# Kernel tuning notes

Hardware: AMD Instinct MI355X
Metric: run time of the kernel (lower is better)

Reference implementation:

```python
import jax, jax.numpy as jnp
import numpy as np

N_NODES = 100000
EPS = 1e-5


def _layernorm(x, gamma, beta):
    mu = jnp.mean(x, axis=-1, keepdims=True)
    var = jnp.mean(jnp.square(x - mu), axis=-1, keepdims=True)
    return (x - mu) * jax.lax.rsqrt(var + EPS) * gamma + beta


def _gcn_layer(src, dst, feat, gamma, beta, W, b):
    # copy_u + sum: aggregate source features into destination nodes
    agg = jax.ops.segment_sum(feat[src], dst, num_segments=N_NODES)
    h = _layernorm(agg, gamma, beta)
    return h @ W + b


def setup_inputs() -> dict:
    key = jax.random.key(0)
    ks = jax.random.split(key, 16)
    d_in, d_hid, d_out = 128, 128, 128
    E = 1600000

    def lin(k, fan_in, fan_out):
        kw, kb = jax.random.split(k)
        lim = 1.0 / np.sqrt(fan_in)
        W = jax.random.uniform(kw, (fan_in, fan_out), jnp.float32, -lim, lim)
        b = jax.random.uniform(kb, (fan_out,), jnp.float32, -lim, lim)
        return W, b

    W1, b1 = lin(ks[0], d_in, d_hid)
    W2, b2 = lin(ks[1], d_hid, d_hid)
    W3, b3 = lin(ks[2], d_hid, d_out)
    return {
        "features": jax.random.normal(ks[3], (N_NODES, d_in), jnp.float32),
        "src": jax.random.randint(ks[4], (E,), 0, N_NODES, jnp.int32),
        "dst": jax.random.randint(ks[5], (E,), 0, N_NODES, jnp.int32),
        "g1": jnp.ones((d_in,), jnp.float32), "be1": jnp.zeros((d_in,), jnp.float32),
        "W1": W1, "b1": b1,
        "g2": jnp.ones((d_hid,), jnp.float32), "be2": jnp.zeros((d_hid,), jnp.float32),
        "W2": W2, "b2": b2,
        "g3": jnp.ones((d_hid,), jnp.float32), "be3": jnp.zeros((d_hid,), jnp.float32),
        "W3": W3, "b3": b3,
    }


def reference(features, src, dst, g1, be1, W1, b1, g2, be2, W2, b2, g3, be3, W3, b3):
    x = jax.nn.relu(_gcn_layer(src, dst, features, g1, be1, W1, b1))
    x = jax.nn.relu(_gcn_layer(src, dst, x, g2, be2, W2, b2))
    x = _gcn_layer(src, dst, x, g3, be3, W3, b3)
    return x
```

## Files before the change

kernel.cpp:

```cpp
#include <hip/hip_runtime.h>
#include <hip/hip_bf16.h>
#include <stdint.h>

typedef unsigned short u16;
typedef __attribute__((ext_vector_type(8))) short short8;
typedef __attribute__((ext_vector_type(4))) float f32x4;

#define DIM 128
#define CAP 64

__device__ __forceinline__ float bflo(uint32_t v) {
    uint32_t b = v << 16;
    float f; __builtin_memcpy(&f, &b, 4); return f;
}
__device__ __forceinline__ float bfhi(uint32_t v) {
    uint32_t b = v & 0xffff0000u;
    float f; __builtin_memcpy(&f, &b, 4); return f;
}
__device__ __forceinline__ u16 f2bf(float f) {
    uint32_t x; __builtin_memcpy(&x, &f, 4);
    uint32_t r = (x + 0x7fffu + ((x >> 16) & 1u)) >> 16;
    return (u16)r;
}
__device__ __forceinline__ uint32_t pack2bf(float a, float b) {
    return (uint32_t)f2bf(a) | ((uint32_t)f2bf(b) << 16);
}


__global__ __launch_bounds__(256) void k_bin1(
    const int* __restrict__ src, const int* __restrict__ dst,
    uint32_t* __restrict__ gCur, uint32_t* __restrict__ groupBuf,
    int E, int ngrp, int gcap)
{
    __shared__ uint32_t hcnt[512];
    __shared__ uint32_t hbase[512];
    __shared__ uint32_t hcur[512];
    int nb = gridDim.x;
    int per = (E + nb - 1) / nb;
    int lo = blockIdx.x * per;
    int hi = lo + per; if (hi > E) hi = E;

    for (int t = threadIdx.x; t < ngrp; t += 256) { hcnt[t] = 0; hcur[t] = 0; }
    __syncthreads();

    for (int i = lo + threadIdx.x; i < hi; i += 256)
        atomicAdd(&hcnt[((uint32_t)dst[i]) >> 8], 1u);
    __syncthreads();

    int rot = (blockIdx.x * 37) % (ngrp > 0 ? ngrp : 1);
    for (int k = threadIdx.x; k < ngrp; k += 256) {
        int t = k + rot; if (t >= ngrp) t -= ngrp;
        uint32_t c = hcnt[t];
        hbase[t] = c ? atomicAdd(&gCur[t], c) : 0u;
    }
    __syncthreads();

    for (int i = lo + threadIdx.x; i < hi; i += 256) {
        uint32_t d = (uint32_t)dst[i];
        uint32_t g = d >> 8;
        uint32_t off = hbase[g] + atomicAdd(&hcur[g], 1u);
        if (off < (uint32_t)gcap)
            groupBuf[(size_t)g * gcap + off] = (uint32_t)src[i] | ((d & 255u) << 20);
    }
}

__global__ __launch_bounds__(256) void k_bin2(
    const uint32_t* __restrict__ groupBuf, const uint32_t* __restrict__ gCur,
    uint32_t* __restrict__ bucket, uint32_t* __restrict__ cnt,
    int N, int gcap)
{
    __shared__ uint32_t ncur[256];
    int g = blockIdx.x;
    ncur[threadIdx.x] = 0;
    __syncthreads();
    uint32_t m = gCur[g]; if (m > (uint32_t)gcap) m = gcap;
    int nodebase = g << 8;
    const uint32_t* buf = groupBuf + (size_t)g * gcap;
    for (uint32_t i = threadIdx.x; i < m; i += 256) {
        uint32_t v = buf[i];
        uint32_t nl = v >> 20;
        uint32_t s = v & 0xFFFFFu;
        uint32_t pos = atomicAdd(&ncur[nl], 1u);
        if (pos < CAP) bucket[(size_t)(nodebase + (int)nl) * CAP + pos] = s;
    }
    __syncthreads();
    int node = nodebase + threadIdx.x;
    if (node < N) cnt[node] = ncur[threadIdx.x];
}


__global__ void k_cast(const float* __restrict__ in, uint32_t* __restrict__ out, int n4) {
    int i = blockIdx.x * blockDim.x + threadIdx.x;
    int stride = gridDim.x * blockDim.x;
    const float4* in4 = (const float4*)in;
    uint2* out2 = (uint2*)out;
    for (; i < n4; i += stride) {
        float4 v = in4[i];
        uint2 r;
        r.x = pack2bf(v.x, v.y);
        r.y = pack2bf(v.z, v.w);
        out2[i] = r;
    }
}


__global__ void k_zero_row(uint32_t* __restrict__ a, uint32_t* __restrict__ b, int N) {
    int t = threadIdx.x;
    if (t < 64) a[(size_t)N * 64 + t] = 0u;
    else        b[(size_t)N * 64 + (t - 64)] = 0u;
}


__global__ void k_transpose3(const float* __restrict__ w0, const float* __restrict__ w1,
                             const float* __restrict__ w2, u16* __restrict__ t0,
                             u16* __restrict__ t1, u16* __restrict__ t2) {
    const float* w = blockIdx.x == 0 ? w0 : (blockIdx.x == 1 ? w1 : w2);
    u16* o = blockIdx.x == 0 ? t0 : (blockIdx.x == 1 ? t1 : t2);
    for (int idx = threadIdx.x; idx < DIM * DIM; idx += blockDim.x) {
        int r = idx >> 7, c = idx & 127;
        o[c * DIM + r] = f2bf(w[idx]);
    }
}


__global__ __launch_bounds__(256) void k_gather_ln(
    const uint32_t* __restrict__ xin, const uint32_t* __restrict__ cnt,
    const uint32_t* __restrict__ bucket,
    const int* __restrict__ src, const int* __restrict__ dst,
    const float* __restrict__ gamma, const float* __restrict__ beta,
    uint32_t* __restrict__ h, int N, int E)
{
    int w = threadIdx.x >> 6, l = threadIdx.x & 63;
    int node = __builtin_amdgcn_readfirstlane(blockIdx.x * 4 + w);
    if (node >= N) return;
    uint32_t c = cnt[node];
    float a0 = 0.f, a1 = 0.f;

    if (__builtin_expect(c > CAP, 0)) {
        for (int e = 0; e < E; ++e) {
            if (dst[e] == node) {
                uint32_t v = xin[(size_t)src[e] * 64 + l];
                a0 += bflo(v); a1 += bfhi(v);
            }
        }
    } else {
        uint32_t bktv = bucket[(size_t)node * CAP + l];
#pragma unroll
        for (int g = 0; g < 4; ++g) {
            if ((uint32_t)(g * 16 + 16) <= c) {
                uint32_t v[16];
#pragma unroll
                for (int i = 0; i < 16; ++i) {
                    const int SLOT = g * 16 + i;
                    uint32_t su = (uint32_t)__builtin_amdgcn_readfirstlane(
                        (int)((uint32_t)__builtin_amdgcn_readlane(bktv, SLOT)));
                    v[i] = (xin + (size_t)su * 64)[l];
                }
#pragma unroll
                for (int i = 0; i < 16; ++i) { a0 += bflo(v[i]); a1 += bfhi(v[i]); }
            } else if ((uint32_t)(g * 16) < c) {
                uint32_t v[16];
#pragma unroll
                for (int q = 0; q < 4; ++q) {
                    if ((uint32_t)(g * 16 + q * 4) < c) {
#pragma unroll
                        for (int i = 0; i < 4; ++i) {
                            const int SLOT = g * 16 + q * 4 + i;
                            uint32_t su = (uint32_t)__builtin_amdgcn_readfirstlane(
                                (int)((uint32_t)__builtin_amdgcn_readlane(bktv, SLOT)));
                            su = ((uint32_t)SLOT < c) ? su : (uint32_t)N;
                            v[q * 4 + i] = (xin + (size_t)su * 64)[l];
                        }
                    }
                }
#pragma unroll
                for (int q = 0; q < 4; ++q) {
                    if ((uint32_t)(g * 16 + q * 4) < c) {
#pragma unroll
                        for (int i = 0; i < 4; ++i) {
                            a0 += bflo(v[q * 4 + i]); a1 += bfhi(v[q * 4 + i]);
                        }
                    }
                }
            }
        }
    }

    float sum = a0 + a1;
    float sq  = a0 * a0 + a1 * a1;
    for (int off = 32; off; off >>= 1) {
        sum += __shfl_xor(sum, off, 64);
        sq  += __shfl_xor(sq,  off, 64);
    }
    float mean = sum * (1.f / 128.f);
    float var  = sq * (1.f / 128.f) - mean * mean;
    float rs   = rsqrtf(var + 1e-5f);
    float g0 = gamma[2 * l], g1 = gamma[2 * l + 1];
    float b0 = beta[2 * l],  b1 = beta[2 * l + 1];
    float h0 = (a0 - mean) * rs * g0 + b0;
    float h1 = (a1 - mean) * rs * g1 + b1;
    h[(size_t)node * 64 + l] = pack2bf(h0, h1);
}


template <int RELU, int OUTF32>
__global__ __launch_bounds__(256) void k_gemm(
    const u16* __restrict__ h, const u16* __restrict__ wt,
    const float* __restrict__ bias, void* __restrict__ outp, int N)
{
    int w = threadIdx.x >> 6, l = threadIdx.x & 63;
    int colbase = (w >> 1) * 64;
    int lr = l & 15, lg = l >> 4;

    short8 bfrag[4][4];
    float bv[4];
#pragma unroll
    for (int ct = 0; ct < 4; ++ct) {
        bv[ct] = bias[colbase + ct * 16 + lr];
#pragma unroll
        for (int kc = 0; kc < 4; ++kc)
            bfrag[ct][kc] = *(const short8*)(wt + (size_t)(colbase + ct * 16 + lr) * DIM + kc * 32 + lg * 8);
    }

    int ntiles = (N + 31) / 32;
    int t = blockIdx.x;
    if (t >= ntiles) return;

    auto loadA = [&](int tt, short8* af) {
        int ar = tt * 32 + 16 * (w & 1) + lr;
        if (ar > N - 1) ar = N - 1;
#pragma unroll
        for (int kc = 0; kc < 4; ++kc)
            af[kc] = *(const short8*)(h + (size_t)ar * DIM + kc * 32 + lg * 8);
    };

    short8 afrag[4];
    loadA(t, afrag);

    while (true) {
        int tn = t + (int)gridDim.x;
        bool has = tn < ntiles;
        short8 anext[4];
        if (has) loadA(tn, anext);

        int row0 = t * 32 + 16 * (w & 1);
#pragma unroll
        for (int ct = 0; ct < 4; ++ct) {
            f32x4 a = {0.f, 0.f, 0.f, 0.f};
#pragma unroll
            for (int kc = 0; kc < 4; ++kc)
                a = __builtin_amdgcn_mfma_f32_16x16x32_bf16(afrag[kc], bfrag[ct][kc], a, 0, 0, 0);
            int col = colbase + ct * 16 + lr;
#pragma unroll
            for (int j = 0; j < 4; ++j) {
                int row = row0 + lg * 4 + j;
                float v = a[j] + bv[ct];
                if (RELU) v = fmaxf(v, 0.f);
                if (row < N) {
                    if (OUTF32) ((float*)outp)[(size_t)row * DIM + col] = v;
                    else        ((u16*)outp)[(size_t)row * DIM + col] = f2bf(v);
                }
            }
        }

        if (!has) break;
#pragma unroll
        for (int kc = 0; kc < 4; ++kc) afrag[kc] = anext[kc];
        t = tn;
    }
}


extern "C" void kernel_launch(void* const* d_in, const int* in_sizes, int n_in,
                              void* d_out, int out_size, void* d_ws, size_t ws_size,
                              hipStream_t stream) {
    const float* feat = (const float*)d_in[0];
    const int* src  = (const int*)d_in[1];
    const int* dst  = (const int*)d_in[2];
    const float* g1 = (const float*)d_in[3],  *be1 = (const float*)d_in[4];
    const float* W1 = (const float*)d_in[5],  *b1  = (const float*)d_in[6];
    const float* g2 = (const float*)d_in[7],  *be2 = (const float*)d_in[8];
    const float* W2 = (const float*)d_in[9],  *b2  = (const float*)d_in[10];
    const float* g3 = (const float*)d_in[11], *be3 = (const float*)d_in[12];
    const float* W3 = (const float*)d_in[13], *b3  = (const float*)d_in[14];

    int N = in_sizes[0] / DIM;
    int E = in_sizes[1];
    float* out = (float*)d_out;

    int ngrp = (N + 255) >> 8;
    int gcap = (E / (ngrp > 0 ? ngrp : 1)) * 3 / 2 + 1024;

    char* ws = (char*)d_ws;
    auto alloc = [&](size_t bytes) {
        char* p = ws;
        ws += (bytes + 255) & ~(size_t)255;
        return p;
    };
    uint32_t* gCur     = (uint32_t*)alloc((size_t)ngrp * 4);
    uint32_t* groupBuf = (uint32_t*)alloc((size_t)ngrp * gcap * 4);
    uint32_t* cnt      = (uint32_t*)alloc((size_t)N * 4);
    uint32_t* bucket   = (uint32_t*)alloc((size_t)N * CAP * 4);
    u16* wt1 = (u16*)alloc(DIM * DIM * 2);
    u16* wt2 = (u16*)alloc(DIM * DIM * 2);
    u16* wt3 = (u16*)alloc(DIM * DIM * 2);
    uint32_t* X0 = (uint32_t*)alloc((size_t)(N + 1) * 64 * 4);
    uint32_t* H  = (uint32_t*)alloc((size_t)(N + 1) * 64 * 4);
    uint32_t* X  = (uint32_t*)alloc((size_t)(N + 1) * 64 * 4);

    hipMemsetAsync(gCur, 0, (size_t)ngrp * 4, stream);
    k_bin1<<<256, 256, 0, stream>>>(src, dst, gCur, groupBuf, E, ngrp, gcap);
    k_bin2<<<ngrp, 256, 0, stream>>>(groupBuf, gCur, bucket, cnt, N, gcap);
    k_transpose3<<<3, 256, 0, stream>>>(W1, W2, W3, wt1, wt2, wt3);
    k_cast<<<1024, 256, 0, stream>>>(feat, X0, N * 32);
    k_zero_row<<<1, 128, 0, stream>>>(X0, X, N);

    int gblocks = (N + 3) / 4;

    k_gather_ln<<<gblocks, 256, 0, stream>>>(X0, cnt, bucket, src, dst, g1, be1, H, N, E);
    k_gemm<1, 0><<<512, 256, 0, stream>>>((const u16*)H, wt1, b1, X, N);
    k_gather_ln<<<gblocks, 256, 0, stream>>>(X, cnt, bucket, src, dst, g2, be2, H, N, E);
    k_gemm<1, 0><<<512, 256, 0, stream>>>((const u16*)H, wt2, b2, X, N);
    k_gather_ln<<<gblocks, 256, 0, stream>>>(X, cnt, bucket, src, dst, g3, be3, H, N, E);
    k_gemm<0, 1><<<512, 256, 0, stream>>>((const u16*)H, wt3, b3, out, N);
}
```

Before: 310.0 us.

## Process two nodes per wavefront in gather-LN and merge prep kernels

The gather+layernorm kernel now has each wavefront aggregate two destination nodes, issuing two independent sets of gathers to raise memory-level parallelism. The warp reductions for both nodes are interleaved. The tail handling is simplified to always issue 16 loads per group, with unused slots redirected to the zero row. The weight-transpose, cast and zero-row kernels are fused into one prep launch to cut launch overhead, and k_bin1 gets twice as many blocks. The risks are higher register pressure, fewer waves in flight, and wasted loads on partial groups.

```diff
diff --git a/kernel.cpp b/kernel.cpp
--- a/kernel.cpp
+++ b/kernel.cpp
@@ -89,36 +89,37 @@
 }
 
 
-__global__ void k_cast(const float* __restrict__ in, uint32_t* __restrict__ out, int n4) {
-    int i = blockIdx.x * blockDim.x + threadIdx.x;
-    int stride = gridDim.x * blockDim.x;
-    const float4* in4 = (const float4*)in;
-    uint2* out2 = (uint2*)out;
-    for (; i < n4; i += stride) {
-        float4 v = in4[i];
-        uint2 r;
-        r.x = pack2bf(v.x, v.y);
-        r.y = pack2bf(v.z, v.w);
-        out2[i] = r;
-    }
-}
-
-
-__global__ void k_zero_row(uint32_t* __restrict__ a, uint32_t* __restrict__ b, int N) {
-    int t = threadIdx.x;
-    if (t < 64) a[(size_t)N * 64 + t] = 0u;
-    else        b[(size_t)N * 64 + (t - 64)] = 0u;
-}
-
-
-__global__ void k_transpose3(const float* __restrict__ w0, const float* __restrict__ w1,
-                             const float* __restrict__ w2, u16* __restrict__ t0,
-                             u16* __restrict__ t1, u16* __restrict__ t2) {
-    const float* w = blockIdx.x == 0 ? w0 : (blockIdx.x == 1 ? w1 : w2);
-    u16* o = blockIdx.x == 0 ? t0 : (blockIdx.x == 1 ? t1 : t2);
-    for (int idx = threadIdx.x; idx < DIM * DIM; idx += blockDim.x) {
-        int r = idx >> 7, c = idx & 127;
-        o[c * DIM + r] = f2bf(w[idx]);
+__global__ void k_prep(const float* __restrict__ feat, uint32_t* __restrict__ X0,
+                       uint32_t* __restrict__ X, int N,
+                       const float* __restrict__ W1, const float* __restrict__ W2,
+                       const float* __restrict__ W3,
+                       u16* __restrict__ t0, u16* __restrict__ t1, u16* __restrict__ t2)
+{
+    int b = blockIdx.x;
+    if (b < 3) {
+        const float* w = b == 0 ? W1 : (b == 1 ? W2 : W3);
+        u16* o = b == 0 ? t0 : (b == 1 ? t1 : t2);
+        for (int idx = threadIdx.x; idx < DIM * DIM; idx += blockDim.x) {
+            int r = idx >> 7, c = idx & 127;
+            o[c * DIM + r] = f2bf(w[idx]);
+        }
+    } else if (b == 3) {
+        int t = threadIdx.x;
+        if (t < 64) X0[(size_t)N * 64 + t] = 0u;
+        else if (t < 128) X[(size_t)N * 64 + (t - 64)] = 0u;
+    } else {
+        int n4 = N * 32;
+        int i = (b - 4) * 256 + threadIdx.x;
+        int stride = (gridDim.x - 4) * 256;
+        const float4* in4 = (const float4*)feat;
+        uint2* out2 = (uint2*)X0;
+        for (; i < n4; i += stride) {
+            float4 v = in4[i];
+            uint2 r;
+            r.x = pack2bf(v.x, v.y);
+            r.y = pack2bf(v.z, v.w);
+            out2[i] = r;
+        }
     }
 }
 
@@ -131,75 +132,85 @@
     uint32_t* __restrict__ h, int N, int E)
 {
     int w = threadIdx.x >> 6, l = threadIdx.x & 63;
-    int node = __builtin_amdgcn_readfirstlane(blockIdx.x * 4 + w);
-    if (node >= N) return;
-    uint32_t c = cnt[node];
-    float a0 = 0.f, a1 = 0.f;
-
-    if (__builtin_expect(c > CAP, 0)) {
+    int node0 = __builtin_amdgcn_readfirstlane(2 * (blockIdx.x * 4 + w));
+    if (node0 >= N) return;
+    int node1 = node0 + 1;
+    bool has1 = node1 < N;
+    uint32_t c0 = cnt[node0];
+    uint32_t c1 = has1 ? cnt[node1] : 0u;
+    float a0 = 0.f, a1 = 0.f, b0 = 0.f, b1 = 0.f;
+
+    if (__builtin_expect(c0 > CAP || c1 > CAP, 0)) {
         for (int e = 0; e < E; ++e) {
-            if (dst[e] == node) {
-                uint32_t v = xin[(size_t)src[e] * 64 + l];
-                a0 += bflo(v); a1 += bfhi(v);
-            }
+            int d = dst[e];
+            if (d == node0) { uint32_t v = xin[(size_t)src[e] * 64 + l]; a0 += bflo(v); a1 += bfhi(v); }
+            else if (d == node1) { uint32_t v = xin[(size_t)src[e] * 64 + l]; b0 += bflo(v); b1 += bfhi(v); }
         }
     } else {
-        uint32_t bktv = bucket[(size_t)node * CAP + l];
-#pragma unroll
-        for (int g = 0; g < 4; ++g) {
-            if ((uint32_t)(g * 16 + 16) <= c) {
-                uint32_t v[16];
-#pragma unroll
-                for (int i = 0; i < 16; ++i) {
-                    const int SLOT = g * 16 + i;
-                    uint32_t su = (uint32_t)__builtin_amdgcn_readfirstlane(
-                        (int)((uint32_t)__builtin_amdgcn_readlane(bktv, SLOT)));
-                    v[i] = (xin + (size_t)su * 64)[l];
-                }
-#pragma unroll
-                for (int i = 0; i < 16; ++i) { a0 += bflo(v[i]); a1 += bfhi(v[i]); }
-            } else if ((uint32_t)(g * 16) < c) {
-                uint32_t v[16];
-#pragma unroll
-                for (int q = 0; q < 4; ++q) {
-                    if ((uint32_t)(g * 16 + q * 4) < c) {
-#pragma unroll
-                        for (int i = 0; i < 4; ++i) {
-                            const int SLOT = g * 16 + q * 4 + i;
-                            uint32_t su = (uint32_t)__builtin_amdgcn_readfirstlane(
-                                (int)((uint32_t)__builtin_amdgcn_readlane(bktv, SLOT)));
-                            su = ((uint32_t)SLOT < c) ? su : (uint32_t)N;
-                            v[q * 4 + i] = (xin + (size_t)su * 64)[l];
-                        }
+        {
+            uint32_t bktv = bucket[(size_t)node0 * CAP + l];
+#pragma unroll
+            for (int g = 0; g < 4; ++g) {
+                if ((uint32_t)(g * 16) < c0) {
+                    uint32_t v[16];
+#pragma unroll
+                    for (int i = 0; i < 16; ++i) {
+                        const int SLOT = g * 16 + i;
+                        uint32_t su = (uint32_t)__builtin_amdgcn_readfirstlane(
+                            (int)((uint32_t)__builtin_amdgcn_readlane(bktv, SLOT)));
+                        su = ((uint32_t)SLOT < c0) ? su : (uint32_t)N;
+                        v[i] = (xin + (size_t)su * 64)[l];
                     }
-                }
-#pragma unroll
-                for (int q = 0; q < 4; ++q) {
-                    if ((uint32_t)(g * 16 + q * 4) < c) {
-#pragma unroll
-                        for (int i = 0; i < 4; ++i) {
-                            a0 += bflo(v[q * 4 + i]); a1 += bfhi(v[q * 4 + i]);
-                        }
-                    }
+#pragma unroll
+                    for (int i = 0; i < 16; ++i) { a0 += bflo(v[i]); a1 += bfhi(v[i]); }
                 }
             }
         }
-    }
-
-    float sum = a0 + a1;
-    float sq  = a0 * a0 + a1 * a1;
+        if (has1) {
+            uint32_t bktv = bucket[(size_t)node1 * CAP + l];
+#pragma unroll
+            for (int g = 0; g < 4; ++g) {
+                if ((uint32_t)(g * 16) < c1) {
+                    uint32_t v[16];
+#pragma unroll
+                    for (int i = 0; i < 16; ++i) {
+                        const int SLOT = g * 16 + i;
+                        uint32_t su = (uint32_t)__builtin_amdgcn_readfirstlane(
+                            (int)((uint32_t)__builtin_amdgcn_readlane(bktv, SLOT)));
+                        su = ((uint32_t)SLOT < c1) ? su : (uint32_t)N;
+                        v[i] = (xin + (size_t)su * 64)[l];
+                    }
+#pragma unroll
+                    for (int i = 0; i < 16; ++i) { b0 += bflo(v[i]); b1 += bfhi(v[i]); }
+                }
+            }
+        }
+    }
+
+    float sA = a0 + a1, qA = a0 * a0 + a1 * a1;
+    float sB = b0 + b1, qB = b0 * b0 + b1 * b1;
     for (int off = 32; off; off >>= 1) {
-        sum += __shfl_xor(sum, off, 64);
-        sq  += __shfl_xor(sq,  off, 64);
-    }
-    float mean = sum * (1.f / 128.f);
-    float var  = sq * (1.f / 128.f) - mean * mean;
-    float rs   = rsqrtf(var + 1e-5f);
-    float g0 = gamma[2 * l], g1 = gamma[2 * l + 1];
-    float b0 = beta[2 * l],  b1 = beta[2 * l + 1];
-    float h0 = (a0 - mean) * rs * g0 + b0;
-    float h1 = (a1 - mean) * rs * g1 + b1;
-    h[(size_t)node * 64 + l] = pack2bf(h0, h1);
+        sA += __shfl_xor(sA, off, 64);
+        sB += __shfl_xor(sB, off, 64);
+        qA += __shfl_xor(qA, off, 64);
+        qB += __shfl_xor(qB, off, 64);
+    }
+    float gg0 = gamma[2 * l], gg1 = gamma[2 * l + 1];
+    float bb0 = beta[2 * l],  bb1 = beta[2 * l + 1];
+    {
+        float mean = sA * (1.f / 128.f);
+        float var  = qA * (1.f / 128.f) - mean * mean;
+        float rs   = rsqrtf(var + 1e-5f);
+        h[(size_t)node0 * 64 + l] =
+            pack2bf((a0 - mean) * rs * gg0 + bb0, (a1 - mean) * rs * gg1 + bb1);
+    }
+    if (has1) {
+        float mean = sB * (1.f / 128.f);
+        float var  = qB * (1.f / 128.f) - mean * mean;
+        float rs   = rsqrtf(var + 1e-5f);
+        h[(size_t)node1 * 64 + l] =
+            pack2bf((b0 - mean) * rs * gg0 + bb0, (b1 - mean) * rs * gg1 + bb1);
+    }
 }
 
 
@@ -290,6 +301,7 @@
 
     int ngrp = (N + 255) >> 8;
     int gcap = (E / (ngrp > 0 ? ngrp : 1)) * 3 / 2 + 1024;
+    int npair = (N + 1) / 2;
 
     char* ws = (char*)d_ws;
     auto alloc = [&](size_t bytes) {
@@ -309,13 +321,11 @@
     uint32_t* X  = (uint32_t*)alloc((size_t)(N + 1) * 64 * 4);
 
     hipMemsetAsync(gCur, 0, (size_t)ngrp * 4, stream);
-    k_bin1<<<256, 256, 0, stream>>>(src, dst, gCur, groupBuf, E, ngrp, gcap);
+    k_bin1<<<512, 256, 0, stream>>>(src, dst, gCur, groupBuf, E, ngrp, gcap);
     k_bin2<<<ngrp, 256, 0, stream>>>(groupBuf, gCur, bucket, cnt, N, gcap);
-    k_transpose3<<<3, 256, 0, stream>>>(W1, W2, W3, wt1, wt2, wt3);
-    k_cast<<<1024, 256, 0, stream>>>(feat, X0, N * 32);
-    k_zero_row<<<1, 128, 0, stream>>>(X0, X, N);
-
-    int gblocks = (N + 3) / 4;
+    k_prep<<<1028, 256, 0, stream>>>(feat, X0, X, N, W1, W2, W3, wt1, wt2, wt3);
+
+    int gblocks = (npair + 3) / 4;
 
     k_gather_ln<<<gblocks, 256, 0, stream>>>(X0, cnt, bucket, src, dst, g1, be1, H, N, E);
     k_gemm<1, 0><<<512, 256, 0, stream>>>((const u16*)H, wt1, b1, X, N);
```

Result: no change. 305.4 us (-1.5%).
